# Optimization experiments

Hardware: AMD Instinct MI355X
Metric: run time of the kernel (lower is better)

## Reference

```python
import jax, jax.numpy as jnp
import numpy as np

B, T, D = 256, 2048, 64

def setup_inputs() -> dict:
    key = jax.random.key(0)
    k1, k2 = jax.random.split(key)
    x = jax.random.normal(k1, (B, T, D), dtype=jnp.float32)
    W = jax.random.normal(k2, (D, D), dtype=jnp.float32)
    b = jnp.zeros((T, D), dtype=jnp.float32)
    return {"x": x, "W": W, "b": b}

def reference(x, W, b):
    # e = tanh(x @ W + b): [B,T,D]
    e = jnp.tanh(jnp.einsum('btd,de->bte', x, W) + b)
    # softmax over time axis (axis=1)
    a = jax.nn.softmax(e, axis=1)
    # return_sequences=True -> elementwise reweighted sequence
    return x * a
```

## Files before the change

kernel.cpp:

```cpp
#include <hip/hip_runtime.h>

typedef __attribute__((ext_vector_type(8))) short short8;
typedef __attribute__((ext_vector_type(4))) float f32x4;
typedef __attribute__((ext_vector_type(4))) unsigned int uint4v;

#define B_SZ 256
#define T_SZ 2048
#define D_SZ 64
#define TILES_PER_WAVE 4
#define SEGS 8
#define APAD 68

__device__ __forceinline__ unsigned int bf16_hi_bits(float f) {
    return (__float_as_uint(f) + 0x8000u) & 0xffff0000u;
}

template <bool LO>
__device__ __forceinline__ void split8(const float4 a, const float4 b,
                                       short8& hi, short8& lo) {
    const float v[8] = {a.x, a.y, a.z, a.w, b.x, b.y, b.z, b.w};
    unsigned int h[4], l[4];
#pragma unroll
    for (int i = 0; i < 8; i += 2) {
        const unsigned int h0 = bf16_hi_bits(v[i]);
        const unsigned int h1 = bf16_hi_bits(v[i + 1]);
        h[i >> 1] = (h0 >> 16) | (h1 & 0xffff0000u);
        if (LO) {
            const float l0 = v[i] - __uint_as_float(h0);
            const float l1 = v[i + 1] - __uint_as_float(h1);
            l[i >> 1] = ((__float_as_uint(l0) + 0x8000u) >> 16) |
                        ((__float_as_uint(l1) + 0x8000u) & 0xffff0000u);
        }
    }
    const uint4v hu = {h[0], h[1], h[2], h[3]};
    hi = __builtin_bit_cast(short8, hu);
    if (LO) {
        const uint4v lu = {l[0], l[1], l[2], l[3]};
        lo = __builtin_bit_cast(short8, lu);
    }
}

__device__ __forceinline__ float exp_tanh(float e) {
    const float u = __expf(2.0f * e);
    const float rr = __builtin_amdgcn_rcpf(1.0f + u);
    return __expf(1.0f - 2.0f * rr);
}

__global__ __launch_bounds__(256) void tca_prep(const float* __restrict__ W,
                                                unsigned int* __restrict__ Wf,
                                                float* __restrict__ S) {
    const int tid = threadIdx.x;
    const float4 z = make_float4(0.f, 0.f, 0.f, 0.f);
    ((float4*)S)[blockIdx.x * 256 + tid] = z;

    if (blockIdx.x != 0) return;
#pragma unroll
    for (int u = 0; u < 4; ++u) {
        const int lf = tid + u * 256;
        const int f = lf >> 6;
        const int lane = lf & 63;
        const int h = f >> 3;
        const int nb = (f & 7) >> 1;
        const int kb = f & 1;
        const int col = nb * 16 + (lane & 15);
        const int krow = kb * 32 + (lane >> 4) * 8;
        unsigned int d[4];
#pragma unroll
        for (int i = 0; i < 8; i += 2) {
            const float w0 = W[(krow + i) * D_SZ + col];
            const float w1 = W[(krow + i + 1) * D_SZ + col];
            unsigned int b0, b1;
            if (h == 0) {
                b0 = bf16_hi_bits(w0);
                b1 = bf16_hi_bits(w1);
            } else {
                const float l0 = w0 - __uint_as_float(bf16_hi_bits(w0));
                const float l1 = w1 - __uint_as_float(bf16_hi_bits(w1));
                b0 = (__float_as_uint(l0) + 0x8000u) & 0xffff0000u;
                b1 = (__float_as_uint(l1) + 0x8000u) & 0xffff0000u;
            }
            d[i >> 1] = (b0 >> 16) | (b1 & 0xffff0000u);
        }
        const uint4v dv = {d[0], d[1], d[2], d[3]};
        ((uint4v*)Wf)[f * 64 + lane] = dv;
    }
}

__global__ __launch_bounds__(256, 8) void tca_colsum(
        const float* __restrict__ x, const unsigned int* __restrict__ Wf,
        const float* __restrict__ bias, float* __restrict__ S) {
    __shared__ uint4v wf_lds[8 * 64];

    const int tid = threadIdx.x;
    const int wave = tid >> 6;
    const int lane = tid & 63;
    const int b = blockIdx.x >> 3;
    const int seg = blockIdx.x & (SEGS - 1);

#pragma unroll
    for (int q = 0; q < 2; ++q)
        wf_lds[tid + q * 256] = ((const uint4v*)Wf)[tid + q * 256];
    __syncthreads();

    const int arow = lane & 15;
    const int aoff = (lane >> 4) * 8;
    const int crow = (lane >> 4) * 4;
    const int ccol = lane & 15;

    float csum[4] = {0.f, 0.f, 0.f, 0.f};
    const int t_wave = seg * 256 + wave * 64;

#pragma unroll 1
    for (int tile = 0; tile < TILES_PER_WAVE; ++tile) {
        const int t0 = t_wave + tile * 16;
        const float* xrow = x + ((size_t)b * T_SZ + t0 + arow) * D_SZ + aoff;
        const float4 xa0 = *(const float4*)(xrow);
        const float4 xa1 = *(const float4*)(xrow + 4);
        const float4 xb0 = *(const float4*)(xrow + 32);
        const float4 xb1 = *(const float4*)(xrow + 36);

        short8 ah[2], dummy;
        split8<false>(xa0, xa1, ah[0], dummy);
        split8<false>(xb0, xb1, ah[1], dummy);

        f32x4 c[4];
#pragma unroll
        for (int nb = 0; nb < 4; ++nb) {
            f32x4 acc = {0.f, 0.f, 0.f, 0.f};
#pragma unroll
            for (int kb = 0; kb < 2; ++kb) {
                const short8 whf = __builtin_bit_cast(short8, wf_lds[(nb * 2 + kb) * 64 + lane]);
                acc = __builtin_amdgcn_mfma_f32_16x16x32_bf16(ah[kb], whf, acc, 0, 0, 0);
            }
            c[nb] = acc;
        }

        const float* brow = bias + (size_t)(t0 + crow) * D_SZ + ccol;
#pragma unroll
        for (int nb = 0; nb < 4; ++nb)
#pragma unroll
            for (int r = 0; r < 4; ++r)
                csum[nb] += exp_tanh(c[nb][r] + brow[r * D_SZ + nb * 16]);
    }

#pragma unroll
    for (int nb = 0; nb < 4; ++nb) {
        float v = csum[nb];
        v += __shfl_xor(v, 16, 64);
        v += __shfl_xor(v, 32, 64);
        if (lane < 16) atomicAdd(&S[b * D_SZ + nb * 16 + lane], v);
    }
}

__global__ __launch_bounds__(256, 4) void tca_out(
        const float* __restrict__ x, const unsigned int* __restrict__ Wf,
        const float* __restrict__ bias, const float* __restrict__ S,
        float* __restrict__ out) {
    __shared__ uint4v wf_lds[16 * 64];
    __shared__ float a_lds[4][16 * APAD];

    const int tid = threadIdx.x;
    const int wave = tid >> 6;
    const int lane = tid & 63;
    const int b = blockIdx.x >> 3;
    const int seg = blockIdx.x & (SEGS - 1);

#pragma unroll
    for (int q = 0; q < 4; ++q)
        wf_lds[tid + q * 256] = ((const uint4v*)Wf)[tid + q * 256];
    __syncthreads();

    const int arow = lane & 15;
    const int aoff = (lane >> 4) * 8;
    const int crow = (lane >> 4) * 4;
    const int ccol = lane & 15;
    const int erow = lane >> 4;
    const int ecol = (lane & 15) * 4;

    float rcpS[4];
#pragma unroll
    for (int nb = 0; nb < 4; ++nb)
        rcpS[nb] = __builtin_amdgcn_rcpf(S[b * D_SZ + nb * 16 + ccol]);

    const int t_wave = seg * 256 + wave * 64;

#pragma unroll 1
    for (int tile = 0; tile < TILES_PER_WAVE; ++tile) {
        const int t0 = t_wave + tile * 16;
        const float* xrow = x + ((size_t)b * T_SZ + t0 + arow) * D_SZ + aoff;
        const float4 xa0 = *(const float4*)(xrow);
        const float4 xa1 = *(const float4*)(xrow + 4);
        const float4 xb0 = *(const float4*)(xrow + 32);
        const float4 xb1 = *(const float4*)(xrow + 36);

        short8 ah[2], al[2];
        split8<true>(xa0, xa1, ah[0], al[0]);
        split8<true>(xb0, xb1, ah[1], al[1]);

        f32x4 c[4];
#pragma unroll
        for (int nb = 0; nb < 4; ++nb) {
            f32x4 acc = {0.f, 0.f, 0.f, 0.f};
#pragma unroll
            for (int kb = 0; kb < 2; ++kb) {
                const short8 whf = __builtin_bit_cast(short8, wf_lds[(nb * 2 + kb) * 64 + lane]);
                const short8 wlf = __builtin_bit_cast(short8, wf_lds[(8 + nb * 2 + kb) * 64 + lane]);
                acc = __builtin_amdgcn_mfma_f32_16x16x32_bf16(ah[kb], whf, acc, 0, 0, 0);
                acc = __builtin_amdgcn_mfma_f32_16x16x32_bf16(ah[kb], wlf, acc, 0, 0, 0);
                acc = __builtin_amdgcn_mfma_f32_16x16x32_bf16(al[kb], whf, acc, 0, 0, 0);
            }
            c[nb] = acc;
        }

        const float* brow = bias + (size_t)(t0 + crow) * D_SZ + ccol;
#pragma unroll
        for (int nb = 0; nb < 4; ++nb)
#pragma unroll
            for (int r = 0; r < 4; ++r)
                a_lds[wave][(crow + r) * APAD + nb * 16 + ccol] =
                    exp_tanh(c[nb][r] + brow[r * D_SZ + nb * 16]) * rcpS[nb];

        const size_t gbase = ((size_t)b * T_SZ + t0) * D_SZ;
#pragma unroll
        for (int j = 0; j < 4; ++j) {
            const int row = j * 4 + erow;
            const float4 av = *(const float4*)&a_lds[wave][row * APAD + ecol];
            const float4 xv = *(const float4*)(x + gbase + row * D_SZ + ecol);
            float4 o;
            o.x = xv.x * av.x; o.y = xv.y * av.y;
            o.z = xv.z * av.z; o.w = xv.w * av.w;
            *(float4*)(out + gbase + row * D_SZ + ecol) = o;
        }
    }
}

extern "C" void kernel_launch(void* const* d_in, const int* in_sizes, int n_in,
                              void* d_out, int out_size, void* d_ws, size_t ws_size,
                              hipStream_t stream) {
    const float* x = (const float*)d_in[0];
    const float* W = (const float*)d_in[1];
    const float* bias = (const float*)d_in[2];
    float* out = (float*)d_out;

    unsigned int* Wf = (unsigned int*)d_ws;
    float* S = (float*)d_ws + 4096;

    tca_prep<<<16, 256, 0, stream>>>(W, Wf, S);

    const dim3 grid(B_SZ * SEGS);
    const dim3 block(256);
    tca_colsum<<<grid, block, 0, stream>>>(x, Wf, bias, S);
    tca_out<<<grid, block, 0, stream>>>(x, Wf, bias, S, out);
}
```

Measured before the change: 91.22 us.

## Fuse column-sum and output kernels into one block-per-batch kernel

```diff
diff --git a/kernel.cpp b/kernel.cpp
--- a/kernel.cpp
+++ b/kernel.cpp
@@ -7,8 +7,8 @@
 #define B_SZ 256
 #define T_SZ 2048
 #define D_SZ 64
-#define TILES_PER_WAVE 4
-#define SEGS 8
+#define WAVES 16
+#define TILES 8
 #define APAD 68
 
 __device__ __forceinline__ unsigned int bf16_hi_bits(float f) {
@@ -47,13 +47,8 @@
 }
 
 __global__ __launch_bounds__(256) void tca_prep(const float* __restrict__ W,
-                                                unsigned int* __restrict__ Wf,
-                                                float* __restrict__ S) {
+                                                unsigned int* __restrict__ Wf) {
     const int tid = threadIdx.x;
-    const float4 z = make_float4(0.f, 0.f, 0.f, 0.f);
-    ((float4*)S)[blockIdx.x * 256 + tid] = z;
-
-    if (blockIdx.x != 0) return;
 #pragma unroll
     for (int u = 0; u < 4; ++u) {
         const int lf = tid + u * 256;
@@ -86,32 +81,34 @@
     }
 }
 
-__global__ __launch_bounds__(256, 8) void tca_colsum(
+__global__ __launch_bounds__(1024, 4) void tca_fused(
         const float* __restrict__ x, const unsigned int* __restrict__ Wf,
-        const float* __restrict__ bias, float* __restrict__ S) {
-    __shared__ uint4v wf_lds[8 * 64];
+        const float* __restrict__ bias, float* __restrict__ out) {
+    __shared__ uint4v wf_lds[16 * 64];
+    __shared__ float a_lds[WAVES][16 * APAD];
+    __shared__ float red[WAVES][64];
+    __shared__ float rcpS_lds[64];
 
     const int tid = threadIdx.x;
     const int wave = tid >> 6;
     const int lane = tid & 63;
-    const int b = blockIdx.x >> 3;
-    const int seg = blockIdx.x & (SEGS - 1);
-
-#pragma unroll
-    for (int q = 0; q < 2; ++q)
-        wf_lds[tid + q * 256] = ((const uint4v*)Wf)[tid + q * 256];
+    const int b = blockIdx.x;
+
+    wf_lds[tid] = ((const uint4v*)Wf)[tid];
     __syncthreads();
 
     const int arow = lane & 15;
     const int aoff = (lane >> 4) * 8;
     const int crow = (lane >> 4) * 4;
     const int ccol = lane & 15;
+    const int erow = lane >> 4;
+    const int ecol = (lane & 15) * 4;
+
+    const int t_wave = wave * (T_SZ / WAVES);
 
     float csum[4] = {0.f, 0.f, 0.f, 0.f};
-    const int t_wave = seg * 256 + wave * 64;
-
 #pragma unroll 1
-    for (int tile = 0; tile < TILES_PER_WAVE; ++tile) {
+    for (int tile = 0; tile < TILES; ++tile) {
         const int t0 = t_wave + tile * 16;
         const float* xrow = x + ((size_t)b * T_SZ + t0 + arow) * D_SZ + aoff;
         const float4 xa0 = *(const float4*)(xrow);
@@ -148,44 +145,25 @@
         float v = csum[nb];
         v += __shfl_xor(v, 16, 64);
         v += __shfl_xor(v, 32, 64);
-        if (lane < 16) atomicAdd(&S[b * D_SZ + nb * 16 + lane], v);
-    }
-}
-
-__global__ __launch_bounds__(256, 4) void tca_out(
-        const float* __restrict__ x, const unsigned int* __restrict__ Wf,
-        const float* __restrict__ bias, const float* __restrict__ S,
-        float* __restrict__ out) {
-    __shared__ uint4v wf_lds[16 * 64];
-    __shared__ float a_lds[4][16 * APAD];
-
-    const int tid = threadIdx.x;
-    const int wave = tid >> 6;
-    const int lane = tid & 63;
-    const int b = blockIdx.x >> 3;
-    const int seg = blockIdx.x & (SEGS - 1);
-
-#pragma unroll
-    for (int q = 0; q < 4; ++q)
-        wf_lds[tid + q * 256] = ((const uint4v*)Wf)[tid + q * 256];
+        if (lane < 16) red[wave][nb * 16 + lane] = v;
+    }
     __syncthreads();
 
-    const int arow = lane & 15;
-    const int aoff = (lane >> 4) * 8;
-    const int crow = (lane >> 4) * 4;
-    const int ccol = lane & 15;
-    const int erow = lane >> 4;
-    const int ecol = (lane & 15) * 4;
+    if (tid < 64) {
+        float s = 0.f;
+#pragma unroll
+        for (int w = 0; w < WAVES; ++w) s += red[w][tid];
+        rcpS_lds[tid] = __builtin_amdgcn_rcpf(s);
+    }
+    __syncthreads();
 
     float rcpS[4];
 #pragma unroll
     for (int nb = 0; nb < 4; ++nb)
-        rcpS[nb] = __builtin_amdgcn_rcpf(S[b * D_SZ + nb * 16 + ccol]);
-
-    const int t_wave = seg * 256 + wave * 64;
+        rcpS[nb] = rcpS_lds[nb * 16 + ccol];
 
 #pragma unroll 1
-    for (int tile = 0; tile < TILES_PER_WAVE; ++tile) {
+    for (int tile = 0; tile < TILES; ++tile) {
         const int t0 = t_wave + tile * 16;
         const float* xrow = x + ((size_t)b * T_SZ + t0 + arow) * D_SZ + aoff;
         const float4 xa0 = *(const float4*)(xrow);
@@ -243,12 +221,7 @@
     float* out = (float*)d_out;
 
     unsigned int* Wf = (unsigned int*)d_ws;
-    float* S = (float*)d_ws + 4096;
-
-    tca_prep<<<16, 256, 0, stream>>>(W, Wf, S);
-
-    const dim3 grid(B_SZ * SEGS);
-    const dim3 block(256);
-    tca_colsum<<<grid, block, 0, stream>>>(x, Wf, bias, S);
-    tca_out<<<grid, block, 0, stream>>>(x, Wf, bias, S, out);
-}
+
+    tca_prep<<<1, 256, 0, stream>>>(W, Wf);
+    tca_fused<<<B_SZ, 1024, 0, stream>>>(x, Wf, bias, out);
+}
```

After: 92.20 us. Within noise of the previous version (+1.1%).
